# Kernel optimization log

Measured on AMD Instinct MI355X. Metric: run time of the kernel, lower is better.

## Reference

```python
import jax, jax.numpy as jnp
import numpy as np

BN_EPS = 1e-5
DIST_MIN = 1e-10


def _three_nn(p1t, p2t):
    # p1t: [B,N,3], p2t: [B,S,3] -> squared dists/idx of 3 nearest, [B,N,3]
    d2 = (jnp.sum(p1t * p1t, -1, keepdims=True)
          - 2.0 * jnp.einsum('bnc,bsc->bns', p1t, p2t)
          + jnp.sum(p2t * p2t, -1)[:, None, :])  # [B,N,S]
    neg, idx = jax.lax.top_k(-d2, 3)
    return -neg, idx


def _gather_knn(f2t, idx):
    # f2t: [B,S,D], idx: [B,N,3] -> [B,N,3,D]
    return jax.vmap(lambda f, i: f[i])(f2t, idx)


def _conv_bn_relu(x, W, b, g, beta):
    # x: [B,C,N]; 1x1 conv == channel GEMM, then train-mode BN, then ReLU
    y = jnp.einsum('oc,bcn->bon', W, x) + b[None, :, None]
    mean = jnp.mean(y, axis=(0, 2), keepdims=True)
    var = jnp.mean((y - mean) ** 2, axis=(0, 2), keepdims=True)
    yn = (y - mean) * jax.lax.rsqrt(var + BN_EPS)
    return jax.nn.relu(yn * g[None, :, None] + beta[None, :, None])


def setup_inputs() -> dict:
    key = jax.random.key(0)
    ks = jax.random.split(key, 10)
    B, N, S, D1, D2 = 4, 8192, 2048, 128, 256
    C_in, C_mid, C_out = D1 + D2, 256, 256
    inp = {
        'pos1': jax.random.normal(ks[0], (B, 3, N), jnp.float32),
        'pos2': jax.random.normal(ks[1], (B, 3, S), jnp.float32),
        'feature1': jax.random.normal(ks[2], (B, D1, N), jnp.float32),
        'feature2': jax.random.normal(ks[3], (B, D2, S), jnp.float32),
        'W1': jax.random.normal(ks[4], (C_mid, C_in), jnp.float32) / np.sqrt(C_in),
        'b1': jnp.zeros((C_mid,), jnp.float32),
        'g1': jnp.ones((C_mid,), jnp.float32),
        'beta1': jnp.zeros((C_mid,), jnp.float32),
        'W2': jax.random.normal(ks[5], (C_out, C_mid), jnp.float32) / np.sqrt(C_mid),
        'b2': jnp.zeros((C_out,), jnp.float32),
        'g2': jnp.ones((C_out,), jnp.float32),
        'beta2': jnp.zeros((C_out,), jnp.float32),
    }
    return inp


def reference(pos1, pos2, feature1, feature2, W1, b1, g1, beta1, W2, b2, g2, beta2):
    B = pos1.shape[0]
    p1t = jnp.transpose(pos1, (0, 2, 1))  # [B,N,3]
    p2t = jnp.transpose(pos2, (0, 2, 1))  # [B,S,3]
    dists, idx = _three_nn(p1t, p2t)      # [B,N,3]
    dists = jnp.maximum(dists, DIST_MIN)
    w = 1.0 / dists
    w = w / jnp.sum(w, -1, keepdims=True)  # [B,N,3]
    f2t = jnp.transpose(feature2, (0, 2, 1))  # [B,S,D2]
    gathered = _gather_knn(f2t, idx)           # [B,N,3,D2]
    interp = jnp.sum(gathered * w[..., None], axis=2)  # [B,N,D2]
    interp = jnp.transpose(interp, (0, 2, 1))          # [B,D2,N]
    feat = jnp.concatenate([interp, feature1], axis=1)  # [B,D2+D1,N]
    feat = _conv_bn_relu(feat, W1, b1, g1, beta1)
    feat = _conv_bn_relu(feat, W2, b2, g2, beta2)
    return feat
```

## Files before the change

kernel.cpp:

```cpp
#include <hip/hip_runtime.h>
#include <hip/hip_bf16.h>

constexpr int B = 4, N = 8192, S = 2048;

typedef __attribute__((ext_vector_type(8))) short short8;
typedef __attribute__((ext_vector_type(4))) float v4f;

__device__ inline float u2f(ushort u) {
    union { ushort u; __hip_bfloat16 h; } c; c.u = u; return __bfloat162float(c.h);
}
__device__ inline ushort f2u(float f) {
    union { ushort u; __hip_bfloat16 h; } c; c.h = __float2bfloat16(f); return c.u;
}
__device__ inline void async_lds16(const void* g, void* l) {
    __builtin_amdgcn_global_load_lds(
        (const __attribute__((address_space(1))) unsigned*)g,
        (__attribute__((address_space(3))) unsigned*)l, 16, 0, 0);
}
__device__ inline short8 ld8(const ushort* p) { return *(const short8*)p; }

__device__ inline void transpose_tile(
    const float* __restrict__ ip, ushort* __restrict__ op,
    int L, int C, int l0, int c0, int tt, ushort (*tl)[66])
{
    const int lr = tt & 63, cb = tt >> 6;
    #pragma unroll
    for (int i = 0; i < 16; ++i) {
        int c = cb + 4 * i;
        tl[lr][c] = f2u(ip[(size_t)(c0 + c) * L + l0 + lr]);
    }
    __syncthreads();
    const int cp = tt & 31, lrow = tt >> 5;
    #pragma unroll
    for (int i = 0; i < 8; ++i) {
        int l = lrow + 8 * i;
        ushort2 v;
        v.x = tl[l][2 * cp]; v.y = tl[l][2 * cp + 1];
        *(ushort2*)(op + (size_t)(l0 + l) * C + c0 + 2 * cp) = v;
    }
}

__global__ __launch_bounds__(512) void prep_all(
    const float* __restrict__ W1, const float* __restrict__ W2,
    const float* __restrict__ pos2, const float* __restrict__ f2,
    const float* __restrict__ f1, const float* __restrict__ pos1,
    ushort* __restrict__ W1r, ushort* __restrict__ W2r,
    float* __restrict__ zero_region,
    ushort* __restrict__ f2T, ushort* __restrict__ f1T,
    float* __restrict__ wgt, int* __restrict__ idxb)
{
    __shared__ __align__(16) char sm[45056];
    const int bid = blockIdx.x;
    const int t = threadIdx.x;

    if (bid < 512) {
        float4* pk = (float4*)sm;
        float*  dL = (float*)(sm + 32768);
        int*    iL = (int*)  (sm + 32768 + 6144);
        const int b = bid >> 7, n0 = (bid & 127) * 64;
        const int lane = t & 63;
        const int w = __builtin_amdgcn_readfirstlane(t >> 6);

        for (int i = t; i < S; i += 512) {
            float x = pos2[(b * 3 + 0) * S + i];
            float y = pos2[(b * 3 + 1) * S + i];
            float z = pos2[(b * 3 + 2) * S + i];
            pk[i] = make_float4(x, y, z, x * x + y * y + z * z);
        }
        __syncthreads();

        {
            const int qi = n0 + lane;
            const float x1 = pos1[(b * 3 + 0) * N + qi];
            const float y1 = pos1[(b * 3 + 1) * N + qi];
            const float z1 = pos1[(b * 3 + 2) * N + qi];
            const float t1 = x1 * x1 + y1 * y1 + z1 * z1;
            const float4* __restrict__ pp = pk + w * 256;
            float d0 = 3.4e38f, d1 = 3.4e38f, d2 = 3.4e38f;
            int i0 = 0x7fffffff, i1 = 0x7fffffff, i2 = 0x7fffffff;
            #pragma unroll 8
            for (int i = 0; i < 256; ++i) {
                float4 p = pp[i];
                float dot = fmaf(x1, p.x, fmaf(y1, p.y, z1 * p.z));
                float dd = fmaf(-2.f, dot, t1) + p.w;
                int s = w * 256 + i;
                bool c0 = dd < d0, c1 = dd < d1, c2 = dd < d2;
                i2 = c1 ? i1 : (c2 ? s : i2);
                i1 = c0 ? i0 : (c1 ? s : i1);
                i0 = c0 ? s : i0;
                float nd1 = __builtin_amdgcn_fmed3f(dd, d0, d1);
                float nd2 = __builtin_amdgcn_fmed3f(dd, d1, d2);
                d0 = fminf(d0, dd);
                d1 = nd1; d2 = nd2;
            }
            int base = (w * 64 + lane) * 3;
            dL[base + 0] = d0; dL[base + 1] = d1; dL[base + 2] = d2;
            iL[base + 0] = i0; iL[base + 1] = i1; iL[base + 2] = i2;
        }
        __syncthreads();
        if (t < 64) {
            float f0 = dL[t*3+0], fv1 = dL[t*3+1], fv2 = dL[t*3+2];
            int   j0 = iL[t*3+0], j1 = iL[t*3+1], j2 = iL[t*3+2];
            #pragma unroll
            for (int c = 1; c < 8; ++c) {
                int cb = (c * 64 + t) * 3;
                #pragma unroll
                for (int k = 0; k < 3; ++k) {
                    float d = dL[cb + k]; int id = iL[cb + k];
                    bool l0 = (d < f0)  || (d == f0  && id < j0);
                    bool l1 = (d < fv1) || (d == fv1 && id < j1);
                    bool l2 = (d < fv2) || (d == fv2 && id < j2);
                    if (l0)      { fv2 = fv1; j2 = j1; fv1 = f0; j1 = j0; f0 = d; j0 = id; }
                    else if (l1) { fv2 = fv1; j2 = j1; fv1 = d; j1 = id; }
                    else if (l2) { fv2 = d; j2 = id; }
                }
            }
            float w0 = 1.f / fmaxf(f0, 1e-10f);
            float w1 = 1.f / fmaxf(fv1, 1e-10f);
            float w2 = 1.f / fmaxf(fv2, 1e-10f);
            float inv = 1.f / (w0 + w1 + w2);
            j0 = ((unsigned)j0 < S) ? j0 : 0;
            j1 = ((unsigned)j1 < S) ? j1 : 0;
            j2 = ((unsigned)j2 < S) ? j2 : 0;
            int base = (b * N + n0 + t) * 3;
            wgt[base + 0] = w0 * inv; wgt[base + 1] = w1 * inv; wgt[base + 2] = w2 * inv;
            idxb[base + 0] = j0; idxb[base + 1] = j1; idxb[base + 2] = j2;
        }
    } else if (bid < 768) {
        ushort (*tl)[66] = (ushort(*)[66])(sm + (t >> 8) * 16896);
        const int tt = t & 255;
        int tile = (bid - 512) * 2 + (t >> 8);
        int b = tile >> 7, ct = (tile >> 5) & 3, st = tile & 31;
        transpose_tile(f2 + (size_t)b * 256 * S, f2T + (size_t)b * S * 256,
                       S, 256, st * 64, ct * 64, tt, tl);
    } else if (bid < 1280) {
        ushort (*tl)[66] = (ushort(*)[66])(sm + (t >> 8) * 16896);
        const int tt = t & 255;
        int u = (bid - 768) * 2 + (t >> 8);
        int b = u >> 8, ct = (u >> 7) & 1, lt = u & 127;
        transpose_tile(f1 + (size_t)b * 128 * N, f1T + (size_t)b * N * 128,
                       N, 128, lt * 64, ct * 64, tt, tl);
    } else {
        int i = (bid - 1280) * 512 + t;
        if (i < 12288) {
            int kk = i >> 10, qq = (i >> 8) & 3, o = i & 255;
            const float* src = W1 + o * 384 + kk * 32 + qq * 8;
            float4 a = *(const float4*)src, bb = *(const float4*)(src + 4);
            union { short8 s; ushort u[8]; } pkv;
            pkv.u[0]=f2u(a.x); pkv.u[1]=f2u(a.y); pkv.u[2]=f2u(a.z); pkv.u[3]=f2u(a.w);
            pkv.u[4]=f2u(bb.x); pkv.u[5]=f2u(bb.y); pkv.u[6]=f2u(bb.z); pkv.u[7]=f2u(bb.w);
            *(short8*)(W1r + i * 8) = pkv.s;
        } else if (i < 20480) {
            int u = i - 12288;
            int kk = u >> 10, qq = (u >> 8) & 3, o = u & 255;
            const float* src = W2 + o * 256 + kk * 32 + qq * 8;
            float4 a = *(const float4*)src, bb = *(const float4*)(src + 4);
            union { short8 s; ushort u[8]; } pkv;
            pkv.u[0]=f2u(a.x); pkv.u[1]=f2u(a.y); pkv.u[2]=f2u(a.z); pkv.u[3]=f2u(a.w);
            pkv.u[4]=f2u(bb.x); pkv.u[5]=f2u(bb.y); pkv.u[6]=f2u(bb.z); pkv.u[7]=f2u(bb.w);
            *(short8*)(W2r + u * 8) = pkv.s;
        } else if (i < 21504) {
            zero_region[i - 20480] = 0.f;
        }
    }
}

__global__ __launch_bounds__(512) void gemm1_kernel(
    const ushort* __restrict__ W1r, const float* __restrict__ bias1,
    const ushort* __restrict__ f2T, const ushort* __restrict__ f1T,
    const int* __restrict__ idxb, const float* __restrict__ wgt,
    ushort* __restrict__ y, float* __restrict__ sums)
{
    __shared__ __align__(16) char smem[81920];
    ushort* Xs   = (ushort*)smem;
    ushort* Wbuf = (ushort*)(smem + 49152);

    const int t = threadIdx.x;
    const int lane = t & 63;
    const int w = __builtin_amdgcn_readfirstlane(t >> 6);
    const int b = blockIdx.y;
    const int n0 = blockIdx.x * 64;
    const int q = lane >> 4, r = lane & 15, r7 = r & 7;

    #pragma unroll
    for (int jj = 0; jj < 2; ++jj)
        async_lds16((const char*)W1r + jj * 8192 + t * 16,
                    (char*)Wbuf + jj * 8192 + w * 1024);

    {
        const int lp = t & 31, ro = t >> 5;
        #pragma unroll
        for (int it = 0; it < 4; ++it) {
            int rr = ro + 16 * it;
            int base = (b * N + n0 + rr) * 3;
            int s0 = idxb[base], s1 = idxb[base + 1], s2 = idxb[base + 2];
            s0 = ((unsigned)s0 < S) ? s0 : 0;
            s1 = ((unsigned)s1 < S) ? s1 : 0;
            s2 = ((unsigned)s2 < S) ? s2 : 0;
            float w0 = wgt[base], w1 = wgt[base + 1], w2 = wgt[base + 2];
            union { short8 s; ushort u[8]; } a, c, d, o;
            a.s = ld8(f2T + ((size_t)b * S + s0) * 256 + 8 * lp);
            c.s = ld8(f2T + ((size_t)b * S + s1) * 256 + 8 * lp);
            d.s = ld8(f2T + ((size_t)b * S + s2) * 256 + 8 * lp);
            #pragma unroll
            for (int j = 0; j < 8; ++j)
                o.u[j] = f2u(w0 * u2f(a.u[j]) + w1 * u2f(c.u[j]) + w2 * u2f(d.u[j]));
            *(short8*)(Xs + rr * 384 + ((lp ^ (rr & 7)) * 8)) = o.s;
        }
    }
    {
        const int lp = t & 15, ro = t >> 4;
        #pragma unroll
        for (int it = 0; it < 2; ++it) {
            int rr = ro + 32 * it;
            short8 v = ld8(f1T + ((size_t)b * N + n0 + rr) * 128 + 8 * lp);
            int c = 32 + lp;
            *(short8*)(Xs + rr * 384 + ((c ^ (rr & 7)) * 8)) = v;
        }
    }
    __syncthreads();

    v4f acc[2][4];
    #pragma unroll
    for (int mt = 0; mt < 2; ++mt)
        #pragma unroll
        for (int nf = 0; nf < 4; ++nf) acc[mt][nf] = (v4f){0.f, 0.f, 0.f, 0.f};

    for (int kk = 0; kk < 12; ++kk) {
        if (kk < 11) {
            const char* g = (const char*)W1r + (kk + 1) * 16384;
            char* l = (char*)Wbuf + ((kk + 1) & 1) * 16384;
            #pragma unroll
            for (int jj = 0; jj < 2; ++jj)
                async_lds16(g + jj * 8192 + t * 16, l + jj * 8192 + w * 1024);
        }
        const ushort* Wb = Wbuf + (kk & 1) * 8192;
        short8 af[2], bf[4];
        #pragma unroll
        for (int mt = 0; mt < 2; ++mt)
            af[mt] = ld8(Wb + q * 2048 + (w * 32 + mt * 16 + r) * 8);
        #pragma unroll
        for (int nf = 0; nf < 4; ++nf)
            bf[nf] = ld8(Xs + (nf * 16 + r) * 384 + (((kk * 4 + q) ^ r7) * 8));
        #pragma unroll
        for (int mt = 0; mt < 2; ++mt)
            #pragma unroll
            for (int nf = 0; nf < 4; ++nf)
                acc[mt][nf] = __builtin_amdgcn_mfma_f32_16x16x32_bf16(
                    af[mt], bf[nf], acc[mt][nf], 0, 0, 0);
        __syncthreads();
    }

    float* statS = (float*)Xs;
    float* statQ = statS + 256;
    #pragma unroll
    for (int mt = 0; mt < 2; ++mt) {
        int ob = w * 32 + mt * 16 + q * 4;
        float4 bi = *(const float4*)(bias1 + ob);
        float sj0 = 0, sj1 = 0, sj2 = 0, sj3 = 0;
        float qj0 = 0, qj1 = 0, qj2 = 0, qj3 = 0;
        #pragma unroll
        for (int nf = 0; nf < 4; ++nf) {
            int n = n0 + nf * 16 + r;
            float v0 = acc[mt][nf][0] + bi.x, v1 = acc[mt][nf][1] + bi.y;
            float v2 = acc[mt][nf][2] + bi.z, v3 = acc[mt][nf][3] + bi.w;
            ushort4 pk; pk.x = f2u(v0); pk.y = f2u(v1); pk.z = f2u(v2); pk.w = f2u(v3);
            *(ushort4*)(y + ((size_t)b * N + n) * 256 + ob) = pk;
            sj0 += v0; sj1 += v1; sj2 += v2; sj3 += v3;
            qj0 += v0 * v0; qj1 += v1 * v1; qj2 += v2 * v2; qj3 += v3 * v3;
        }
        #pragma unroll
        for (int m = 1; m <= 8; m <<= 1) {
            sj0 += __shfl_xor(sj0, m); sj1 += __shfl_xor(sj1, m);
            sj2 += __shfl_xor(sj2, m); sj3 += __shfl_xor(sj3, m);
            qj0 += __shfl_xor(qj0, m); qj1 += __shfl_xor(qj1, m);
            qj2 += __shfl_xor(qj2, m); qj3 += __shfl_xor(qj3, m);
        }
        if (r == 0) {
            statS[ob + 0] = sj0; statS[ob + 1] = sj1;
            statS[ob + 2] = sj2; statS[ob + 3] = sj3;
            statQ[ob + 0] = qj0; statQ[ob + 1] = qj1;
            statQ[ob + 2] = qj2; statQ[ob + 3] = qj3;
        }
    }
    __syncthreads();
    if (t < 256) {
        atomicAdd(&sums[t], statS[t]);
        atomicAdd(&sums[256 + t], statQ[t]);
    }
}

__global__ __launch_bounds__(512) void gemm2_kernel(
    const ushort* __restrict__ Wr, const float* __restrict__ bias,
    const float* __restrict__ sums1, const float* __restrict__ g1,
    const float* __restrict__ be1,
    ushort* __restrict__ y, float* __restrict__ sums)
{
    __shared__ __align__(16) ushort Xs[64 * 256];
    __shared__ __align__(16) ushort Wbuf[2 * 8192];
    __shared__ float ssA[256], ssB[256];
    const int t = threadIdx.x;
    const int b = blockIdx.y;
    const int n0 = blockIdx.x * 64;
    const int w = t >> 6, lane = t & 63;
    const int q = lane >> 4, r = lane & 15, r7 = r & 7;

    {
        const char* g0 = (const char*)Wr;
        #pragma unroll
        for (int jj = 0; jj < 2; ++jj)
            async_lds16(g0 + jj * 8192 + t * 16,
                        (char*)Wbuf + jj * 8192 + w * 1024);
    }

    if (t < 256) {
        float sv = sums1[t], qv = sums1[256 + t];
        float mean = sv * (1.f / 32768.f);
        float var = qv * (1.f / 32768.f) - mean * mean;
        float rstd = rsqrtf(var + 1e-5f);
        float sc = g1[t] * rstd;
        ssA[t] = sc;
        ssB[t] = be1[t] - mean * sc;
    }
    __syncthreads();

    {
        const int lp = t & 31, ro = t >> 5;
        #pragma unroll
        for (int it = 0; it < 4; ++it) {
            int rr = ro + 16 * it;
            union { short8 s; ushort u[8]; } v, o;
            v.s = ld8(y + ((size_t)b * N + n0 + rr) * 256 + 8 * lp);
            #pragma unroll
            for (int j = 0; j < 8; ++j)
                o.u[j] = f2u(fmaxf(u2f(v.u[j]) * ssA[8 * lp + j] + ssB[8 * lp + j], 0.f));
            *(short8*)(Xs + rr * 256 + ((lp ^ (rr & 7)) * 8)) = o.s;
        }
    }
    __syncthreads();

    v4f acc[2][4];
    #pragma unroll
    for (int mt = 0; mt < 2; ++mt)
        #pragma unroll
        for (int nf = 0; nf < 4; ++nf) acc[mt][nf] = (v4f){0.f, 0.f, 0.f, 0.f};

    for (int kk = 0; kk < 8; ++kk) {
        if (kk < 7) {
            const char* g = (const char*)Wr + (kk + 1) * 16384;
            char* l = (char*)Wbuf + ((kk + 1) & 1) * 16384;
            #pragma unroll
            for (int jj = 0; jj < 2; ++jj)
                async_lds16(g + jj * 8192 + t * 16, l + jj * 8192 + w * 1024);
        }
        const ushort* Wb = Wbuf + (kk & 1) * 8192;
        short8 af[2], bf[4];
        #pragma unroll
        for (int mt = 0; mt < 2; ++mt)
            af[mt] = ld8(Wb + q * 2048 + (w * 32 + mt * 16 + r) * 8);
        #pragma unroll
        for (int nf = 0; nf < 4; ++nf)
            bf[nf] = ld8(Xs + (nf * 16 + r) * 256 + (((kk * 4 + q) ^ r7) * 8));
        #pragma unroll
        for (int mt = 0; mt < 2; ++mt)
            #pragma unroll
            for (int nf = 0; nf < 4; ++nf)
                acc[mt][nf] = __builtin_amdgcn_mfma_f32_16x16x32_bf16(
                    af[mt], bf[nf], acc[mt][nf], 0, 0, 0);
        __syncthreads();
    }

    float* statS = (float*)Xs;
    float* statQ = statS + 256;
    #pragma unroll
    for (int mt = 0; mt < 2; ++mt) {
        int ob = w * 32 + mt * 16 + q * 4;
        float4 bi = *(const float4*)(bias + ob);
        float sj0 = 0, sj1 = 0, sj2 = 0, sj3 = 0;
        float qj0 = 0, qj1 = 0, qj2 = 0, qj3 = 0;
        #pragma unroll
        for (int nf = 0; nf < 4; ++nf) {
            int n = n0 + nf * 16 + r;
            float v0 = acc[mt][nf][0] + bi.x, v1 = acc[mt][nf][1] + bi.y;
            float v2 = acc[mt][nf][2] + bi.z, v3 = acc[mt][nf][3] + bi.w;
            ushort4 pk; pk.x = f2u(v0); pk.y = f2u(v1); pk.z = f2u(v2); pk.w = f2u(v3);
            *(ushort4*)(y + ((size_t)b * N + n) * 256 + ob) = pk;
            sj0 += v0; sj1 += v1; sj2 += v2; sj3 += v3;
            qj0 += v0 * v0; qj1 += v1 * v1; qj2 += v2 * v2; qj3 += v3 * v3;
        }
        #pragma unroll
        for (int m = 1; m <= 8; m <<= 1) {
            sj0 += __shfl_xor(sj0, m); sj1 += __shfl_xor(sj1, m);
            sj2 += __shfl_xor(sj2, m); sj3 += __shfl_xor(sj3, m);
            qj0 += __shfl_xor(qj0, m); qj1 += __shfl_xor(qj1, m);
            qj2 += __shfl_xor(qj2, m); qj3 += __shfl_xor(qj3, m);
        }
        if (r == 0) {
            statS[ob + 0] = sj0; statS[ob + 1] = sj1;
            statS[ob + 2] = sj2; statS[ob + 3] = sj3;
            statQ[ob + 0] = qj0; statQ[ob + 1] = qj1;
            statQ[ob + 2] = qj2; statQ[ob + 3] = qj3;
        }
    }
    __syncthreads();
    if (t < 256) {
        atomicAdd(&sums[t], statS[t]);
        atomicAdd(&sums[256 + t], statQ[t]);
    }
}

__global__ __launch_bounds__(256) void final_kernel(
    const ushort* __restrict__ Y, const float* __restrict__ sums2,
    const float* __restrict__ g2, const float* __restrict__ be2,
    float* __restrict__ out)
{
    __shared__ float tl[64][65];
    __shared__ float ssA[64], ssB[64];
    const int t = threadIdx.x;
    const int b = blockIdx.z;
    const int n0 = blockIdx.x * 64, c0 = blockIdx.y * 64;

    if (t < 64) {
        int c = c0 + t;
        float sv = sums2[c], qv = sums2[256 + c];
        float mean = sv * (1.f / 32768.f);
        float var = qv * (1.f / 32768.f) - mean * mean;
        float rstd = rsqrtf(var + 1e-5f);
        float sc = g2[c] * rstd;
        ssA[t] = sc;
        ssB[t] = be2[c] - mean * sc;
    }
    __syncthreads();

    const int nl = t >> 3, cho = 8 * (t & 7);
    #pragma unroll
    for (int it = 0; it < 2; ++it) {
        int n = nl + 32 * it;
        union { short8 s; ushort u[8]; } v;
        v.s = ld8(Y + ((size_t)b * N + n0 + n) * 256 + c0 + cho);
        #pragma unroll
        for (int j = 0; j < 8; ++j)
            tl[n][cho + j] = fmaxf(u2f(v.u[j]) * ssA[cho + j] + ssB[cho + j], 0.f);
    }
    __syncthreads();

    const int cl = t >> 4, n4 = (t & 15) * 4;
    #pragma unroll
    for (int it = 0; it < 4; ++it) {
        int c = cl + 16 * it;
        float4 v;
        v.x = tl[n4 + 0][c]; v.y = tl[n4 + 1][c];
        v.z = tl[n4 + 2][c]; v.w = tl[n4 + 3][c];
        *(float4*)(out + ((size_t)b * 256 + c0 + c) * N + n0 + n4) = v;
    }
}

extern "C" void kernel_launch(void* const* d_in, const int* in_sizes, int n_in,
                              void* d_out, int out_size, void* d_ws, size_t ws_size,
                              hipStream_t stream)
{
    (void)in_sizes; (void)n_in; (void)out_size;
    if (ws_size < (30u << 20)) return;

    const float* pos1 = (const float*)d_in[0];
    const float* pos2 = (const float*)d_in[1];
    const float* f1   = (const float*)d_in[2];
    const float* f2   = (const float*)d_in[3];
    const float* W1   = (const float*)d_in[4];
    const float* b1   = (const float*)d_in[5];
    const float* g1   = (const float*)d_in[6];
    const float* be1  = (const float*)d_in[7];
    const float* W2   = (const float*)d_in[8];
    const float* b2   = (const float*)d_in[9];
    const float* g2   = (const float*)d_in[10];
    const float* be2  = (const float*)d_in[11];

    char* ws = (char*)d_ws;
    float*  sums1  = (float*)ws;
    float*  sums2  = sums1 + 512;
    int*    idxb   = (int*)(ws + 4096);
    float*  wgt    = (float*)(ws + 4096 + 393216);
    ushort* W1r    = (ushort*)(ws + 4096 + 786432);
    ushort* W2r    = (ushort*)(ws + 4096 + 786432 + 196608);
    ushort* f2T    = (ushort*)(ws + (2u << 20));
    ushort* f1T    = (ushort*)(ws + (6u << 20));
    ushort* y      = (ushort*)(ws + (14u << 20));

    prep_all<<<1322, 512, 0, stream>>>(W1, W2, pos2, f2, f1, pos1,
                                       W1r, W2r, sums1, f2T, f1T, wgt, idxb);

    gemm1_kernel<<<dim3(N / 64, B), 512, 0, stream>>>(
        W1r, b1, f2T, f1T, idxb, wgt, y, sums1);

    gemm2_kernel<<<dim3(N / 64, B), 512, 0, stream>>>(
        W2r, b2, sums1, g1, be1, y, sums2);

    final_kernel<<<dim3(N / 64, 256 / 64, B), 256, 0, stream>>>(
        y, sums2, g2, be2, (float*)d_out);
}
```

Baseline: 185.7 us.

## Pad LDS strides and single-buffer W1 chunks in gemm1 to cut shared memory

Pads the LDS row strides of the activation tiles (384→392, 256→264) and the per-quarter weight chunk stride (2048→2056) to reduce bank conflicts on MFMA operand loads. In gemm1 the weight buffer becomes single-buffered, which shrinks shared memory from about 80KB to 65KB to allow more resident blocks, but each K-step now waits at two barriers around a synchronous chunk load instead of prefetching. gemm2 keeps double buffering with the padded layout and makes the wave index uniform via readfirstlane.

```diff
diff --git a/kernel.cpp b/kernel.cpp
--- a/kernel.cpp
+++ b/kernel.cpp
@@ -5,6 +5,11 @@
 
 typedef __attribute__((ext_vector_type(8))) short short8;
 typedef __attribute__((ext_vector_type(4))) float v4f;
+
+constexpr int ST1 = 392;
+constexpr int ST2 = 264;
+constexpr int WQ = 2056;
+constexpr int WCH = 8224;
 
 __device__ inline float u2f(ushort u) {
     union { ushort u; __hip_bfloat16 h; } c; c.u = u; return __bfloat162float(c.h);
@@ -18,6 +23,20 @@
         (__attribute__((address_space(3))) unsigned*)l, 16, 0, 0);
 }
 __device__ inline short8 ld8(const ushort* p) { return *(const short8*)p; }
+
+__device__ inline void load_w_chunk(const ushort* Wsrc, int chunk,
+                                    char* WbufDst, int w ,
+                                    int t)
+{
+    const char* g = (const char*)Wsrc + chunk * 16384;
+    #pragma unroll
+    for (int jj = 0; jj < 2; ++jj) {
+        int qq = jj * 2 + (w >> 2);
+        int wl = w & 3;
+        async_lds16(g + qq * 4096 + (t & 255) * 16,
+                    WbufDst + qq * 4112 + wl * 1024);
+    }
+}
 
 __device__ inline void transpose_tile(
     const float* __restrict__ ip, ushort* __restrict__ op,
@@ -171,9 +190,9 @@
     const int* __restrict__ idxb, const float* __restrict__ wgt,
     ushort* __restrict__ y, float* __restrict__ sums)
 {
-    __shared__ __align__(16) char smem[81920];
+    __shared__ __align__(16) char smem[66624];
     ushort* Xs   = (ushort*)smem;
-    ushort* Wbuf = (ushort*)(smem + 49152);
+    char*   Wbuf = smem + 50176;
 
     const int t = threadIdx.x;
     const int lane = t & 63;
@@ -182,10 +201,7 @@
     const int n0 = blockIdx.x * 64;
     const int q = lane >> 4, r = lane & 15, r7 = r & 7;
 
-    #pragma unroll
-    for (int jj = 0; jj < 2; ++jj)
-        async_lds16((const char*)W1r + jj * 8192 + t * 16,
-                    (char*)Wbuf + jj * 8192 + w * 1024);
+    load_w_chunk(W1r, 0, Wbuf, w, t);
 
     {
         const int lp = t & 31, ro = t >> 5;
@@ -205,7 +221,7 @@
             #pragma unroll
             for (int j = 0; j < 8; ++j)
                 o.u[j] = f2u(w0 * u2f(a.u[j]) + w1 * u2f(c.u[j]) + w2 * u2f(d.u[j]));
-            *(short8*)(Xs + rr * 384 + ((lp ^ (rr & 7)) * 8)) = o.s;
+            *(short8*)(Xs + rr * ST1 + ((lp ^ (rr & 7)) * 8)) = o.s;
         }
     }
     {
@@ -215,7 +231,7 @@
             int rr = ro + 32 * it;
             short8 v = ld8(f1T + ((size_t)b * N + n0 + rr) * 128 + 8 * lp);
             int c = 32 + lp;
-            *(short8*)(Xs + rr * 384 + ((c ^ (rr & 7)) * 8)) = v;
+            *(short8*)(Xs + rr * ST1 + ((c ^ (rr & 7)) * 8)) = v;
         }
     }
     __syncthreads();
@@ -227,29 +243,27 @@
         for (int nf = 0; nf < 4; ++nf) acc[mt][nf] = (v4f){0.f, 0.f, 0.f, 0.f};
 
     for (int kk = 0; kk < 12; ++kk) {
-        if (kk < 11) {
-            const char* g = (const char*)W1r + (kk + 1) * 16384;
-            char* l = (char*)Wbuf + ((kk + 1) & 1) * 16384;
-            #pragma unroll
-            for (int jj = 0; jj < 2; ++jj)
-                async_lds16(g + jj * 8192 + t * 16, l + jj * 8192 + w * 1024);
-        }
-        const ushort* Wb = Wbuf + (kk & 1) * 8192;
+        const ushort* Wb = (const ushort*)Wbuf;
         short8 af[2], bf[4];
         #pragma unroll
         for (int mt = 0; mt < 2; ++mt)
-            af[mt] = ld8(Wb + q * 2048 + (w * 32 + mt * 16 + r) * 8);
+            af[mt] = ld8(Wb + q * WQ + (w * 32 + mt * 16 + r) * 8);
         #pragma unroll
         for (int nf = 0; nf < 4; ++nf)
-            bf[nf] = ld8(Xs + (nf * 16 + r) * 384 + (((kk * 4 + q) ^ r7) * 8));
+            bf[nf] = ld8(Xs + (nf * 16 + r) * ST1 + (((kk * 4 + q) ^ r7) * 8));
         #pragma unroll
         for (int mt = 0; mt < 2; ++mt)
             #pragma unroll
             for (int nf = 0; nf < 4; ++nf)
                 acc[mt][nf] = __builtin_amdgcn_mfma_f32_16x16x32_bf16(
                     af[mt], bf[nf], acc[mt][nf], 0, 0, 0);
-        __syncthreads();
-    }
+        if (kk < 11) {
+            __syncthreads();
+            load_w_chunk(W1r, kk + 1, Wbuf, w, t);
+            __syncthreads();
+        }
+    }
+    __syncthreads();
 
     float* statS = (float*)Xs;
     float* statQ = statS + 256;
@@ -296,22 +310,17 @@
     const float* __restrict__ be1,
     ushort* __restrict__ y, float* __restrict__ sums)
 {
-    __shared__ __align__(16) ushort Xs[64 * 256];
-    __shared__ __align__(16) ushort Wbuf[2 * 8192];
+    __shared__ __align__(16) ushort Xs[64 * ST2];
+    __shared__ __align__(16) char Wbuf[2 * 16448];
     __shared__ float ssA[256], ssB[256];
     const int t = threadIdx.x;
     const int b = blockIdx.y;
     const int n0 = blockIdx.x * 64;
-    const int w = t >> 6, lane = t & 63;
+    const int w = __builtin_amdgcn_readfirstlane(t >> 6);
+    const int lane = t & 63;
     const int q = lane >> 4, r = lane & 15, r7 = r & 7;
 
-    {
-        const char* g0 = (const char*)Wr;
-        #pragma unroll
-        for (int jj = 0; jj < 2; ++jj)
-            async_lds16(g0 + jj * 8192 + t * 16,
-                        (char*)Wbuf + jj * 8192 + w * 1024);
-    }
+    load_w_chunk(Wr, 0, Wbuf, w, t);
 
     if (t < 256) {
         float sv = sums1[t], qv = sums1[256 + t];
@@ -334,7 +343,7 @@
             #pragma unroll
             for (int j = 0; j < 8; ++j)
                 o.u[j] = f2u(fmaxf(u2f(v.u[j]) * ssA[8 * lp + j] + ssB[8 * lp + j], 0.f));
-            *(short8*)(Xs + rr * 256 + ((lp ^ (rr & 7)) * 8)) = o.s;
+            *(short8*)(Xs + rr * ST2 + ((lp ^ (rr & 7)) * 8)) = o.s;
         }
     }
     __syncthreads();
@@ -346,21 +355,16 @@
         for (int nf = 0; nf < 4; ++nf) acc[mt][nf] = (v4f){0.f, 0.f, 0.f, 0.f};
 
     for (int kk = 0; kk < 8; ++kk) {
-        if (kk < 7) {
-            const char* g = (const char*)Wr + (kk + 1) * 16384;
-            char* l = (char*)Wbuf + ((kk + 1) & 1) * 16384;
-            #pragma unroll
-            for (int jj = 0; jj < 2; ++jj)
-                async_lds16(g + jj * 8192 + t * 16, l + jj * 8192 + w * 1024);
-        }
-        const ushort* Wb = Wbuf + (kk & 1) * 8192;
+        if (kk < 7)
+            load_w_chunk(Wr, kk + 1, Wbuf + ((kk + 1) & 1) * 16448, w, t);
+        const ushort* Wb = (const ushort*)(Wbuf + (kk & 1) * 16448);
         short8 af[2], bf[4];
         #pragma unroll
         for (int mt = 0; mt < 2; ++mt)
-            af[mt] = ld8(Wb + q * 2048 + (w * 32 + mt * 16 + r) * 8);
+            af[mt] = ld8(Wb + q * WQ + (w * 32 + mt * 16 + r) * 8);
         #pragma unroll
         for (int nf = 0; nf < 4; ++nf)
-            bf[nf] = ld8(Xs + (nf * 16 + r) * 256 + (((kk * 4 + q) ^ r7) * 8));
+            bf[nf] = ld8(Xs + (nf * 16 + r) * ST2 + (((kk * 4 + q) ^ r7) * 8));
         #pragma unroll
         for (int mt = 0; mt < 2; ++mt)
             #pragma unroll
```

Result: no change. 189.4 us (+2.0%).

## Load GEMM weight fragments directly into registers instead of LDS double-buffering

Applied to the files above, without the earlier changes.

Both GEMM kernels now load their full per-wave weight A-fragments from global memory straight into registers at kernel start. This replaces the async global-to-LDS double-buffered pipeline and removes the per-k-step __syncthreads. The K loop is fully unrolled and LDS use drops, with launch-bound occupancy hints added (6 and 8 waves per EU) to allow more resident blocks. The cost is higher register pressure: 24 and 16 short8 fragments per thread. Under the occupancy caps this risks spills, and the weight loads are now exposed latency at kernel start.

```diff
diff --git a/kernel.cpp b/kernel.cpp
--- a/kernel.cpp
+++ b/kernel.cpp
@@ -11,11 +11,6 @@
 }
 __device__ inline ushort f2u(float f) {
     union { ushort u; __hip_bfloat16 h; } c; c.h = __float2bfloat16(f); return c.u;
-}
-__device__ inline void async_lds16(const void* g, void* l) {
-    __builtin_amdgcn_global_load_lds(
-        (const __attribute__((address_space(1))) unsigned*)g,
-        (__attribute__((address_space(3))) unsigned*)l, 16, 0, 0);
 }
 __device__ inline short8 ld8(const ushort* p) { return *(const short8*)p; }
 
@@ -165,15 +160,13 @@
     }
 }
 
-__global__ __launch_bounds__(512) void gemm1_kernel(
+__global__ __launch_bounds__(512, 6) void gemm1_kernel(
     const ushort* __restrict__ W1r, const float* __restrict__ bias1,
     const ushort* __restrict__ f2T, const ushort* __restrict__ f1T,
     const int* __restrict__ idxb, const float* __restrict__ wgt,
     ushort* __restrict__ y, float* __restrict__ sums)
 {
-    __shared__ __align__(16) char smem[81920];
-    ushort* Xs   = (ushort*)smem;
-    ushort* Wbuf = (ushort*)(smem + 49152);
+    __shared__ __align__(16) ushort Xs[64 * 384];
 
     const int t = threadIdx.x;
     const int lane = t & 63;
@@ -182,10 +175,12 @@
     const int n0 = blockIdx.x * 64;
     const int q = lane >> 4, r = lane & 15, r7 = r & 7;
 
-    #pragma unroll
-    for (int jj = 0; jj < 2; ++jj)
-        async_lds16((const char*)W1r + jj * 8192 + t * 16,
-                    (char*)Wbuf + jj * 8192 + w * 1024);
+    short8 af[12][2];
+    #pragma unroll
+    for (int kk = 0; kk < 12; ++kk)
+        #pragma unroll
+        for (int mt = 0; mt < 2; ++mt)
+            af[kk][mt] = ld8(W1r + (kk * 1024 + q * 256 + w * 32 + mt * 16 + r) * 8);
 
     {
         const int lp = t & 31, ro = t >> 5;
@@ -226,19 +221,9 @@
         #pragma unroll
         for (int nf = 0; nf < 4; ++nf) acc[mt][nf] = (v4f){0.f, 0.f, 0.f, 0.f};
 
+    #pragma unroll
     for (int kk = 0; kk < 12; ++kk) {
-        if (kk < 11) {
-            const char* g = (const char*)W1r + (kk + 1) * 16384;
-            char* l = (char*)Wbuf + ((kk + 1) & 1) * 16384;
-            #pragma unroll
-            for (int jj = 0; jj < 2; ++jj)
-                async_lds16(g + jj * 8192 + t * 16, l + jj * 8192 + w * 1024);
-        }
-        const ushort* Wb = Wbuf + (kk & 1) * 8192;
-        short8 af[2], bf[4];
-        #pragma unroll
-        for (int mt = 0; mt < 2; ++mt)
-            af[mt] = ld8(Wb + q * 2048 + (w * 32 + mt * 16 + r) * 8);
+        short8 bf[4];
         #pragma unroll
         for (int nf = 0; nf < 4; ++nf)
             bf[nf] = ld8(Xs + (nf * 16 + r) * 384 + (((kk * 4 + q) ^ r7) * 8));
@@ -247,9 +232,9 @@
             #pragma unroll
             for (int nf = 0; nf < 4; ++nf)
                 acc[mt][nf] = __builtin_amdgcn_mfma_f32_16x16x32_bf16(
-                    af[mt], bf[nf], acc[mt][nf], 0, 0, 0);
-        __syncthreads();
-    }
+                    af[kk][mt], bf[nf], acc[mt][nf], 0, 0, 0);
+    }
+    __syncthreads();
 
     float* statS = (float*)Xs;
     float* statQ = statS + 256;
@@ -290,28 +275,27 @@
     }
 }
 
-__global__ __launch_bounds__(512) void gemm2_kernel(
+__global__ __launch_bounds__(512, 8) void gemm2_kernel(
     const ushort* __restrict__ Wr, const float* __restrict__ bias,
     const float* __restrict__ sums1, const float* __restrict__ g1,
     const float* __restrict__ be1,
     ushort* __restrict__ y, float* __restrict__ sums)
 {
     __shared__ __align__(16) ushort Xs[64 * 256];
-    __shared__ __align__(16) ushort Wbuf[2 * 8192];
     __shared__ float ssA[256], ssB[256];
     const int t = threadIdx.x;
     const int b = blockIdx.y;
     const int n0 = blockIdx.x * 64;
-    const int w = t >> 6, lane = t & 63;
+    const int w = __builtin_amdgcn_readfirstlane(t >> 6);
+    const int lane = t & 63;
     const int q = lane >> 4, r = lane & 15, r7 = r & 7;
 
-    {
-        const char* g0 = (const char*)Wr;
-        #pragma unroll
-        for (int jj = 0; jj < 2; ++jj)
-            async_lds16(g0 + jj * 8192 + t * 16,
-                        (char*)Wbuf + jj * 8192 + w * 1024);
-    }
+    short8 af[8][2];
+    #pragma unroll
+    for (int kk = 0; kk < 8; ++kk)
+        #pragma unroll
+        for (int mt = 0; mt < 2; ++mt)
+            af[kk][mt] = ld8(Wr + (kk * 1024 + q * 256 + w * 32 + mt * 16 + r) * 8);
 
     if (t < 256) {
         float sv = sums1[t], qv = sums1[256 + t];
@@ -345,19 +329,9 @@
         #pragma unroll
         for (int nf = 0; nf < 4; ++nf) acc[mt][nf] = (v4f){0.f, 0.f, 0.f, 0.f};
 
+    #pragma unroll
     for (int kk = 0; kk < 8; ++kk) {
-        if (kk < 7) {
-            const char* g = (const char*)Wr + (kk + 1) * 16384;
-            char* l = (char*)Wbuf + ((kk + 1) & 1) * 16384;
-            #pragma unroll
-            for (int jj = 0; jj < 2; ++jj)
-                async_lds16(g + jj * 8192 + t * 16, l + jj * 8192 + w * 1024);
-        }
-        const ushort* Wb = Wbuf + (kk & 1) * 8192;
-        short8 af[2], bf[4];
-        #pragma unroll
-        for (int mt = 0; mt < 2; ++mt)
-            af[mt] = ld8(Wb + q * 2048 + (w * 32 + mt * 16 + r) * 8);
+        short8 bf[4];
         #pragma unroll
         for (int nf = 0; nf < 4; ++nf)
             bf[nf] = ld8(Xs + (nf * 16 + r) * 256 + (((kk * 4 + q) ^ r7) * 8));
@@ -366,9 +340,9 @@
             #pragma unroll
             for (int nf = 0; nf < 4; ++nf)
                 acc[mt][nf] = __builtin_amdgcn_mfma_f32_16x16x32_bf16(
-                    af[mt], bf[nf], acc[mt][nf], 0, 0, 0);
-        __syncthreads();
-    }
+                    af[kk][mt], bf[nf], acc[mt][nf], 0, 0, 0);
+    }
+    __syncthreads();
 
     float* statS = (float*)Xs;
     float* statQ = statS + 256;
```

Result: slower. 218.4 us (+17.6%).

## Shrink gemm1 LDS via register-staged single W buffer and late feature1 staging

Applied to the files above, without the earlier changes.

Cuts gemm1's shared memory from 80KB to 48KB. The async double-buffered W1 tiles become a single LDS buffer refilled from registers prefetched one k-step ahead. The feature1 slice is loaded into registers early and written into the freed Xs region only after the interpolated-feature k-steps finish, so Xs holds 256 columns instead of 384. The goal is more resident blocks per CU. The cost is two barriers per k-step instead of one and less overlap of W loads with MFMA work.

```diff
diff --git a/kernel.cpp b/kernel.cpp
--- a/kernel.cpp
+++ b/kernel.cpp
@@ -171,9 +171,9 @@
     const int* __restrict__ idxb, const float* __restrict__ wgt,
     ushort* __restrict__ y, float* __restrict__ sums)
 {
-    __shared__ __align__(16) char smem[81920];
-    ushort* Xs   = (ushort*)smem;
-    ushort* Wbuf = (ushort*)(smem + 49152);
+    __shared__ __align__(16) char smem[49152];
+    ushort* Xs = (ushort*)smem;
+    ushort* Wb = (ushort*)(smem + 32768);
 
     const int t = threadIdx.x;
     const int lane = t & 63;
@@ -185,7 +185,13 @@
     #pragma unroll
     for (int jj = 0; jj < 2; ++jj)
         async_lds16((const char*)W1r + jj * 8192 + t * 16,
-                    (char*)Wbuf + jj * 8192 + w * 1024);
+                    (char*)Wb + jj * 8192 + w * 1024);
+
+    short8 f1v[2];
+    const int flp = t & 15, fro = t >> 4;
+    #pragma unroll
+    for (int it = 0; it < 2; ++it)
+        f1v[it] = ld8(f1T + ((size_t)b * N + n0 + fro + 32 * it) * 128 + 8 * flp);
 
     {
         const int lp = t & 31, ro = t >> 5;
@@ -205,17 +211,7 @@
             #pragma unroll
             for (int j = 0; j < 8; ++j)
                 o.u[j] = f2u(w0 * u2f(a.u[j]) + w1 * u2f(c.u[j]) + w2 * u2f(d.u[j]));
-            *(short8*)(Xs + rr * 384 + ((lp ^ (rr & 7)) * 8)) = o.s;
-        }
-    }
-    {
-        const int lp = t & 15, ro = t >> 4;
-        #pragma unroll
-        for (int it = 0; it < 2; ++it) {
-            int rr = ro + 32 * it;
-            short8 v = ld8(f1T + ((size_t)b * N + n0 + rr) * 128 + 8 * lp);
-            int c = 32 + lp;
-            *(short8*)(Xs + rr * 384 + ((c ^ (rr & 7)) * 8)) = v;
+            *(short8*)(Xs + rr * 256 + ((lp ^ (rr & 7)) * 8)) = o.s;
         }
     }
     __syncthreads();
@@ -226,22 +222,17 @@
         #pragma unroll
         for (int nf = 0; nf < 4; ++nf) acc[mt][nf] = (v4f){0.f, 0.f, 0.f, 0.f};
 
-    for (int kk = 0; kk < 12; ++kk) {
-        if (kk < 11) {
-            const char* g = (const char*)W1r + (kk + 1) * 16384;
-            char* l = (char*)Wbuf + ((kk + 1) & 1) * 16384;
-            #pragma unroll
-            for (int jj = 0; jj < 2; ++jj)
-                async_lds16(g + jj * 8192 + t * 16, l + jj * 8192 + w * 1024);
-        }
-        const ushort* Wb = Wbuf + (kk & 1) * 8192;
+    #pragma unroll
+    for (int kk = 0; kk < 8; ++kk) {
+        short8 wreg0 = ld8(W1r + (kk + 1) * 8192 + t * 16);
+        short8 wreg1 = ld8(W1r + (kk + 1) * 8192 + t * 16 + 8);
         short8 af[2], bf[4];
         #pragma unroll
         for (int mt = 0; mt < 2; ++mt)
             af[mt] = ld8(Wb + q * 2048 + (w * 32 + mt * 16 + r) * 8);
         #pragma unroll
         for (int nf = 0; nf < 4; ++nf)
-            bf[nf] = ld8(Xs + (nf * 16 + r) * 384 + (((kk * 4 + q) ^ r7) * 8));
+            bf[nf] = ld8(Xs + (nf * 16 + r) * 256 + (((kk * 4 + q) ^ r7) * 8));
         #pragma unroll
         for (int mt = 0; mt < 2; ++mt)
             #pragma unroll
@@ -249,7 +240,46 @@
                 acc[mt][nf] = __builtin_amdgcn_mfma_f32_16x16x32_bf16(
                     af[mt], bf[nf], acc[mt][nf], 0, 0, 0);
         __syncthreads();
-    }
+        *(short8*)(Wb + t * 16) = wreg0;
+        *(short8*)(Wb + t * 16 + 8) = wreg1;
+        if (kk == 7) {
+            #pragma unroll
+            for (int it = 0; it < 2; ++it) {
+                int rr = fro + 32 * it;
+                *(short8*)(Xs + rr * 128 + ((flp ^ (rr & 7)) * 8)) = f1v[it];
+            }
+        }
+        __syncthreads();
+    }
+
+    #pragma unroll
+    for (int kk = 8; kk < 12; ++kk) {
+        short8 wreg0, wreg1;
+        if (kk < 11) {
+            wreg0 = ld8(W1r + (kk + 1) * 8192 + t * 16);
+            wreg1 = ld8(W1r + (kk + 1) * 8192 + t * 16 + 8);
+        }
+        short8 af[2], bf[4];
+        #pragma unroll
+        for (int mt = 0; mt < 2; ++mt)
+            af[mt] = ld8(Wb + q * 2048 + (w * 32 + mt * 16 + r) * 8);
+        #pragma unroll
+        for (int nf = 0; nf < 4; ++nf)
+            bf[nf] = ld8(Xs + (nf * 16 + r) * 128 + ((((kk - 8) * 4 + q) ^ r7) * 8));
+        #pragma unroll
+        for (int mt = 0; mt < 2; ++mt)
+            #pragma unroll
+            for (int nf = 0; nf < 4; ++nf)
+                acc[mt][nf] = __builtin_amdgcn_mfma_f32_16x16x32_bf16(
+                    af[mt], bf[nf], acc[mt][nf], 0, 0, 0);
+        if (kk < 11) {
+            __syncthreads();
+            *(short8*)(Wb + t * 16) = wreg0;
+            *(short8*)(Wb + t * 16 + 8) = wreg1;
+            __syncthreads();
+        }
+    }
+    __syncthreads();
 
     float* statS = (float*)Xs;
     float* statQ = statS + 256;
```

New measurement: 187.6 us. Within noise of the previous version (+1.0%).
